# Kernel tuning notes

Measured on AMD Instinct MI355X. Metric: run time of the kernel, lower is better.

The kernel has to match this reference:

```python
import jax, jax.numpy as jnp
import numpy as np

EPS = 1e-5  # BatchNorm eps (eval mode, uses running stats)


def _conv1x1(x, W, b):
    # x: [B,C,H,W], W: [O,C], b: [O] -> [B,O,H,W]
    return jnp.einsum('bchw,oc->bohw', x, W) + b[None, :, None, None]


def setup_inputs() -> dict:
    key = jax.random.key(0)
    ks = jax.random.split(key, 13)
    B, C, M, N = 16, 512, 64, 64
    CR = C // 2
    s = 0.02
    return {
        'x': jax.random.normal(ks[0], (B, C, M, N), dtype=jnp.float32),
        'Wq': jax.random.normal(ks[1], (CR, C), dtype=jnp.float32) * s,
        'bq': jax.random.normal(ks[2], (CR,), dtype=jnp.float32) * s,
        'Wk': jax.random.normal(ks[3], (CR, C), dtype=jnp.float32) * s,
        'bk': jax.random.normal(ks[4], (CR,), dtype=jnp.float32) * s,
        'Wv': jax.random.normal(ks[5], (CR, C), dtype=jnp.float32) * s,
        'bv': jax.random.normal(ks[6], (CR,), dtype=jnp.float32) * s,
        'Wr': jax.random.normal(ks[7], (C, CR), dtype=jnp.float32) * s,
        'br': jax.random.normal(ks[8], (C,), dtype=jnp.float32) * s,
        'gamma': jax.random.normal(ks[9], (C,), dtype=jnp.float32) * 0.1 + 1.0,
        'beta': jax.random.normal(ks[10], (C,), dtype=jnp.float32) * 0.1,
        'running_mean': jax.random.normal(ks[11], (C,), dtype=jnp.float32) * 0.1,
        'running_var': jax.random.uniform(ks[12], (C,), dtype=jnp.float32, minval=0.5, maxval=1.5),
    }


def reference(x, Wq, bq, Wk, bk, Wv, bv, Wr, br, gamma, beta, running_mean, running_var):
    b, c, m, n = x.shape
    cr = Wq.shape[0]
    # 1x1-conv QKV projections
    Q = _conv1x1(x, Wq, bq).reshape(b * cr, m, n)
    K = _conv1x1(x, Wk, bk).reshape(b * cr, m, n)
    V = _conv1x1(x, Wv, bv).reshape(b * cr, m, n)
    # per-channel spatial attention over rows: [b*cr, m, m]
    corr = jnp.einsum('gik,gjk->gij', Q, K)
    attn = jax.nn.softmax(corr, axis=-1)
    y = jnp.einsum('gij,gjn->gin', attn, V).reshape(b, cr, m, n)
    # reconstruct: 1x1 conv + BatchNorm (eval mode) + residual
    y = _conv1x1(y, Wr, br)
    inv = gamma / jnp.sqrt(running_var + EPS)
    y = y * inv[None, :, None, None] + (beta - running_mean * inv)[None, :, None, None]
    return y + x
```

## Files before the change

### kernel.cpp

```cpp
#include <hip/hip_runtime.h>

typedef __attribute__((ext_vector_type(8))) short bf16x8;
typedef __attribute__((ext_vector_type(4))) float f32x4;

#define DEVI static __device__ __forceinline__

DEVI unsigned short f2b(float f) {
  union { float f; unsigned u; } v; v.f = f;
  unsigned r = v.u + 0x7fffu + ((v.u >> 16) & 1u);
  return (unsigned short)(r >> 16);
}

typedef const __attribute__((address_space(1))) void* gas1_t;
typedef __attribute__((address_space(3))) void* las3_t;
#define GL16(g, l) __builtin_amdgcn_global_load_lds((gas1_t)(g), (las3_t)(l), 16, 0, 0)

#define WAITVM(N) asm volatile("s_waitcnt vmcnt(" #N ")" ::: "memory")
#define WAITLGKM  asm volatile("s_waitcnt lgkmcnt(0)" ::: "memory")
#define SCHEDBAR  __builtin_amdgcn_sched_barrier(0)

#define OFF_WQKV  0ull
#define OFF_WR    786432ull
#define OFF_BQKV  1048576ull
#define OFF_SCALE 1051648ull
#define OFF_OFF2  1053696ull
#define OFF_XT    2097152ull
#define OFF_YT    2097152ull
#define OFF_Y     35651584ull
#define OFF_Q     69206016ull

__global__ __launch_bounds__(256) void k_xt(
    const float* __restrict__ x, unsigned short* __restrict__ xt,
    const float* __restrict__ Wq, const float* __restrict__ bq,
    const float* __restrict__ Wk, const float* __restrict__ bk,
    const float* __restrict__ Wv, const float* __restrict__ bv,
    const float* __restrict__ Wr, const float* __restrict__ br,
    const float* __restrict__ gamma, const float* __restrict__ beta,
    const float* __restrict__ rm, const float* __restrict__ rv,
    unsigned short* __restrict__ wqkv, unsigned short* __restrict__ wrb,
    float* __restrict__ bqkv, float* __restrict__ scale, float* __restrict__ off2)
{
  __shared__ unsigned short tile[64][72];
  const int t = threadIdx.x;
  const int bid = blockIdx.x + blockIdx.y * 64 + blockIdx.z * 512;

  if (bid < 1536) {
    int i = bid * 256 + t;
    if (i < 768 * 512) {
      int o = i >> 9, c = i & 511;
      float v = (o < 256) ? Wq[o * 512 + c] : (o < 512 ? Wk[(o - 256) * 512 + c] : Wv[(o - 512) * 512 + c]);
      wqkv[i] = f2b(v);
    }
    if (i < 512 * 256) wrb[i] = f2b(Wr[i]);
    if (i < 768) bqkv[i] = (i < 256) ? bq[i] : (i < 512 ? bk[i - 256] : bv[i - 512]);
    if (i < 512) {
      float inv = gamma[i] * rsqrtf(rv[i] + 1e-5f);
      scale[i] = inv;
      off2[i] = (br[i] - rm[i]) * inv + beta[i];
    }
  }

  const int b = blockIdx.z, c0 = blockIdx.y * 64, s0 = blockIdx.x * 64;
  const int r = t >> 2, cc = (t & 3) * 16;
  const float* src = x + ((size_t)b * 512 + c0 + r) * 4096 + s0 + cc;
  #pragma unroll
  for (int j = 0; j < 16; j += 4) {
    float4 v = *(const float4*)(src + j);
    tile[r][cc + j + 0] = f2b(v.x);
    tile[r][cc + j + 1] = f2b(v.y);
    tile[r][cc + j + 2] = f2b(v.z);
    tile[r][cc + j + 3] = f2b(v.w);
  }
  __syncthreads();
  unsigned short* dst = xt + ((size_t)b * 4096 + s0 + r) * 512 + c0 + cc;
  bf16x8 o0, o1;
  #pragma unroll
  for (int j = 0; j < 8; ++j) { o0[j] = tile[cc + j][r]; o1[j] = tile[cc + 8 + j][r]; }
  *(bf16x8*)(dst) = o0;
  *(bf16x8*)(dst + 8) = o1;
}

__global__ __launch_bounds__(256) void k_qkv(
    const unsigned short* __restrict__ xt, const unsigned short* __restrict__ wqkv,
    const float* __restrict__ bqkv, unsigned short* __restrict__ qkv)
{
  __shared__ unsigned short lds[2][2][8192];
  const int wg = (blockIdx.x & 7) * 384 + (blockIdx.x >> 3);
  const int o0 = (wg % 6) * 128;
  const int s0 = ((wg / 6) & 31) * 128;
  const int b  = wg / 192;
  const int t = threadIdx.x, w = t >> 6, l = t & 63;
  const int wm = w >> 1, wn = w & 1, lr = l & 15;
  const int lkE = (l >> 4) * 8;
  const int swE = (lr & 7) * 8;
  const int cp = (t & 7) ^ ((t >> 3) & 7);

  const unsigned short* Ag = wqkv + (size_t)(o0 + (t >> 3)) * 512 + cp * 8;
  const unsigned short* Bg = xt + ((size_t)b * 4096 + s0 + (t >> 3)) * 512 + cp * 8;

  const f32x4 z = {0.f, 0.f, 0.f, 0.f};
  f32x4 acc[4][4];
  #pragma unroll
  for (int i = 0; i < 4; ++i)
    #pragma unroll
    for (int j = 0; j < 4; ++j) acc[i][j] = z;

#define STG_Q(st, kt) do { \
    _Pragma("unroll") \
    for (int j = 0; j < 4; ++j) { \
      GL16(Ag + (kt) * 64 + j * 32 * 512, (char*)&lds[st][0][0] + j * 4096 + t * 16); \
      GL16(Bg + (kt) * 64 + j * 32 * 512, (char*)&lds[st][1][0] + j * 4096 + t * 16); \
    } \
  } while (0)

#define CMP_Q(st) do { \
    const unsigned short* A  = &lds[st][0][0]; \
    const unsigned short* Bl = &lds[st][1][0]; \
    bf16x8 af[2][4], bfr[2][4]; \
    _Pragma("unroll") \
    for (int kc = 0; kc < 2; ++kc) { \
      const int kidx = (kc * 32 + lkE) ^ swE; \
      _Pragma("unroll") \
      for (int mi = 0; mi < 4; ++mi) af[kc][mi] = *(const bf16x8*)(A + (wm * 64 + mi * 16 + lr) * 64 + kidx); \
      _Pragma("unroll") \
      for (int ni = 0; ni < 4; ++ni) bfr[kc][ni] = *(const bf16x8*)(Bl + (wn * 64 + ni * 16 + lr) * 64 + kidx); \
    } \
    __builtin_amdgcn_s_setprio(1); \
    _Pragma("unroll") \
    for (int kc = 0; kc < 2; ++kc) \
      _Pragma("unroll") \
      for (int mi = 0; mi < 4; ++mi) \
        _Pragma("unroll") \
        for (int ni = 0; ni < 4; ++ni) \
          acc[mi][ni] = __builtin_amdgcn_mfma_f32_16x16x32_bf16(af[kc][mi], bfr[kc][ni], acc[mi][ni], 0, 0, 0); \
    __builtin_amdgcn_s_setprio(0); \
  } while (0)

  STG_Q(0, 0); STG_Q(1, 1);
  #pragma unroll
  for (int kt = 0; kt < 7; ++kt) {
    WAITVM(8);
    __builtin_amdgcn_s_barrier(); SCHEDBAR;
    CMP_Q(kt & 1);
    __builtin_amdgcn_s_barrier(); SCHEDBAR;
    if (kt + 2 < 8) STG_Q(kt & 1, kt + 2);
  }
  WAITVM(0);
  __builtin_amdgcn_s_barrier(); SCHEDBAR;
  CMP_Q(1);

  #pragma unroll
  for (int mi = 0; mi < 4; ++mi) {
    #pragma unroll
    for (int reg = 0; reg < 4; ++reg) {
      const int o = o0 + wm * 64 + mi * 16 + (l >> 4) * 4 + reg;
      const float bias = bqkv[o];
      const size_t base = (size_t)(o >> 8) * 16777216ull + ((size_t)b * 256 + (o & 255)) * 4096;
      #pragma unroll
      for (int ni = 0; ni < 4; ++ni) {
        const int s = s0 + wn * 64 + ni * 16 + lr;
        qkv[base + s] = f2b(acc[mi][ni][reg] + bias);
      }
    }
  }
#undef STG_Q
#undef CMP_Q
}

__global__ __launch_bounds__(256) void k_attn(const unsigned short* __restrict__ qkv,
                                              unsigned short* __restrict__ yout)
{
  __shared__ unsigned short Vt[64][80];
  __shared__ unsigned short P[4][16][80];
  const int g = blockIdx.x;
  const unsigned short* qg = qkv + (size_t)g * 4096;
  const unsigned short* kg = qkv + 16777216ull + (size_t)g * 4096;
  const unsigned short* vg = qkv + 33554432ull + (size_t)g * 4096;
  const int t = threadIdx.x, w = t >> 6, l = t & 63;
  const int lr = l & 15, lk = (l >> 4) * 8;

  {
    const int j = t >> 2, c0 = (t & 3) * 16;
    bf16x8 a = *(const bf16x8*)(vg + j * 64 + c0);
    bf16x8 bb = *(const bf16x8*)(vg + j * 64 + c0 + 8);
    #pragma unroll
    for (int jj = 0; jj < 8; ++jj) { Vt[c0 + jj][j] = a[jj]; Vt[c0 + 8 + jj][j] = bb[jj]; }
  }

  const f32x4 z = {0.f, 0.f, 0.f, 0.f};
  bf16x8 qf[2];
  #pragma unroll
  for (int kc = 0; kc < 2; ++kc) qf[kc] = *(const bf16x8*)(qg + (w * 16 + lr) * 64 + kc * 32 + lk);
  f32x4 accS[4] = {z, z, z, z};
  __builtin_amdgcn_s_setprio(1);
  #pragma unroll
  for (int jt = 0; jt < 4; ++jt)
    #pragma unroll
    for (int kc = 0; kc < 2; ++kc) {
      bf16x8 kf = *(const bf16x8*)(kg + (jt * 16 + lr) * 64 + kc * 32 + lk);
      accS[jt] = __builtin_amdgcn_mfma_f32_16x16x32_bf16(qf[kc], kf, accS[jt], 0, 0, 0);
    }
  __builtin_amdgcn_s_setprio(0);

  #pragma unroll
  for (int reg = 0; reg < 4; ++reg) {
    float mx = fmaxf(fmaxf(accS[0][reg], accS[1][reg]), fmaxf(accS[2][reg], accS[3][reg]));
    #pragma unroll
    for (int m = 1; m < 16; m <<= 1) mx = fmaxf(mx, __shfl_xor(mx, m, 64));
    float e0 = __expf(accS[0][reg] - mx), e1 = __expf(accS[1][reg] - mx);
    float e2 = __expf(accS[2][reg] - mx), e3 = __expf(accS[3][reg] - mx);
    float sm = e0 + e1 + e2 + e3;
    #pragma unroll
    for (int m = 1; m < 16; m <<= 1) sm += __shfl_xor(sm, m, 64);
    const float rs = 1.f / sm;
    const int row = (l >> 4) * 4 + reg;
    P[w][row][0 * 16 + lr] = f2b(e0 * rs);
    P[w][row][1 * 16 + lr] = f2b(e1 * rs);
    P[w][row][2 * 16 + lr] = f2b(e2 * rs);
    P[w][row][3 * 16 + lr] = f2b(e3 * rs);
  }
  __syncthreads();

  bf16x8 pf[2];
  #pragma unroll
  for (int kc = 0; kc < 2; ++kc) pf[kc] = *(const bf16x8*)(&P[w][lr][kc * 32 + lk]);
  f32x4 accY[4] = {z, z, z, z};
  __builtin_amdgcn_s_setprio(1);
  #pragma unroll
  for (int nt = 0; nt < 4; ++nt)
    #pragma unroll
    for (int kc = 0; kc < 2; ++kc) {
      bf16x8 vf = *(const bf16x8*)(&Vt[nt * 16 + lr][kc * 32 + lk]);
      accY[nt] = __builtin_amdgcn_mfma_f32_16x16x32_bf16(pf[kc], vf, accY[nt], 0, 0, 0);
    }
  __builtin_amdgcn_s_setprio(0);

  unsigned short* yg = yout + (size_t)g * 4096;
  #pragma unroll
  for (int nt = 0; nt < 4; ++nt)
    #pragma unroll
    for (int reg = 0; reg < 4; ++reg) {
      const int i = w * 16 + (l >> 4) * 4 + reg;
      yg[i * 64 + nt * 16 + lr] = f2b(accY[nt][reg]);
    }
}

__global__ __launch_bounds__(256) void k_yt(const unsigned short* __restrict__ y, unsigned short* __restrict__ yt)
{
  __shared__ unsigned short tile[64][72];
  const int b = blockIdx.z, cr0 = blockIdx.y * 64, s0 = blockIdx.x * 64;
  const int t = threadIdx.x, r = t >> 2, c0 = (t & 3) * 16;
  const unsigned short* src = y + ((size_t)b * 256 + cr0 + r) * 4096 + s0 + c0;
  bf16x8 a = *(const bf16x8*)(src);
  bf16x8 bb = *(const bf16x8*)(src + 8);
  #pragma unroll
  for (int j = 0; j < 8; ++j) { tile[r][c0 + j] = a[j]; tile[r][c0 + 8 + j] = bb[j]; }
  __syncthreads();
  unsigned short* dst = yt + ((size_t)b * 4096 + s0 + r) * 256 + cr0 + c0;
  bf16x8 o0, o1;
  #pragma unroll
  for (int j = 0; j < 8; ++j) { o0[j] = tile[c0 + j][r]; o1[j] = tile[c0 + 8 + j][r]; }
  *(bf16x8*)(dst) = o0;
  *(bf16x8*)(dst + 8) = o1;
}

__global__ __launch_bounds__(256) void k_recon(
    const unsigned short* __restrict__ yt, const unsigned short* __restrict__ wrb,
    const float* __restrict__ scale, const float* __restrict__ off2,
    const float* __restrict__ x, float* __restrict__ out)
{
  __shared__ unsigned short lds[2][2][8192];
  const int wg = (blockIdx.x & 7) * 256 + (blockIdx.x >> 3);
  const int o0 = (wg % 4) * 128;
  const int s0 = ((wg / 4) & 31) * 128;
  const int b  = wg / 128;
  const int t = threadIdx.x, w = t >> 6, l = t & 63;
  const int wm = w >> 1, wn = w & 1, lr = l & 15;
  const int lkE = (l >> 4) * 8;
  const int swE = (lr & 7) * 8;
  const int cp = (t & 7) ^ ((t >> 3) & 7);

  const unsigned short* Ag = wrb + (size_t)(o0 + (t >> 3)) * 256 + cp * 8;
  const unsigned short* Bg = yt + ((size_t)b * 4096 + s0 + (t >> 3)) * 256 + cp * 8;

  const f32x4 z = {0.f, 0.f, 0.f, 0.f};
  f32x4 acc[4][4];
  #pragma unroll
  for (int i = 0; i < 4; ++i)
    #pragma unroll
    for (int j = 0; j < 4; ++j) acc[i][j] = z;

#define STG_R(st, kt) do { \
    _Pragma("unroll") \
    for (int j = 0; j < 4; ++j) { \
      GL16(Ag + (kt) * 64 + j * 32 * 256, (char*)&lds[st][0][0] + j * 4096 + t * 16); \
      GL16(Bg + (kt) * 64 + j * 32 * 256, (char*)&lds[st][1][0] + j * 4096 + t * 16); \
    } \
  } while (0)

#define CMP_R(st) do { \
    const unsigned short* A  = &lds[st][0][0]; \
    const unsigned short* Bl = &lds[st][1][0]; \
    bf16x8 af[2][4], bfr[2][4]; \
    _Pragma("unroll") \
    for (int kc = 0; kc < 2; ++kc) { \
      const int kidx = (kc * 32 + lkE) ^ swE; \
      _Pragma("unroll") \
      for (int mi = 0; mi < 4; ++mi) af[kc][mi] = *(const bf16x8*)(A + (wm * 64 + mi * 16 + lr) * 64 + kidx); \
      _Pragma("unroll") \
      for (int ni = 0; ni < 4; ++ni) bfr[kc][ni] = *(const bf16x8*)(Bl + (wn * 64 + ni * 16 + lr) * 64 + kidx); \
    } \
    __builtin_amdgcn_s_setprio(1); \
    _Pragma("unroll") \
    for (int kc = 0; kc < 2; ++kc) \
      _Pragma("unroll") \
      for (int mi = 0; mi < 4; ++mi) \
        _Pragma("unroll") \
        for (int ni = 0; ni < 4; ++ni) \
          acc[mi][ni] = __builtin_amdgcn_mfma_f32_16x16x32_bf16(af[kc][mi], bfr[kc][ni], acc[mi][ni], 0, 0, 0); \
    __builtin_amdgcn_s_setprio(0); \
  } while (0)

  STG_R(0, 0); STG_R(1, 1);
  #pragma unroll
  for (int kt = 0; kt < 3; ++kt) {
    WAITVM(8);
    __builtin_amdgcn_s_barrier(); SCHEDBAR;
    CMP_R(kt & 1);
    __builtin_amdgcn_s_barrier(); SCHEDBAR;
    if (kt + 2 < 4) STG_R(kt & 1, kt + 2);
  }
  WAITVM(0);
  __builtin_amdgcn_s_barrier(); SCHEDBAR;
  CMP_R(1);

  #pragma unroll
  for (int mi = 0; mi < 4; ++mi) {
    #pragma unroll
    for (int reg = 0; reg < 4; ++reg) {
      const int o = o0 + wm * 64 + mi * 16 + (l >> 4) * 4 + reg;
      const float sc = scale[o], of = off2[o];
      const size_t base = ((size_t)b * 512 + o) * 4096;
      #pragma unroll
      for (int ni = 0; ni < 4; ++ni) {
        const int s = s0 + wn * 64 + ni * 16 + lr;
        const size_t idx = base + s;
        out[idx] = acc[mi][ni][reg] * sc + of + x[idx];
      }
    }
  }
#undef STG_R
#undef CMP_R
}

extern "C" void kernel_launch(void* const* d_in, const int* in_sizes, int n_in,
                              void* d_out, int out_size, void* d_ws, size_t ws_size,
                              hipStream_t stream)
{
  const float* x     = (const float*)d_in[0];
  const float* Wq    = (const float*)d_in[1];
  const float* bq    = (const float*)d_in[2];
  const float* Wk    = (const float*)d_in[3];
  const float* bk    = (const float*)d_in[4];
  const float* Wv    = (const float*)d_in[5];
  const float* bv    = (const float*)d_in[6];
  const float* Wr    = (const float*)d_in[7];
  const float* br    = (const float*)d_in[8];
  const float* gamma = (const float*)d_in[9];
  const float* beta  = (const float*)d_in[10];
  const float* rm    = (const float*)d_in[11];
  const float* rv    = (const float*)d_in[12];

  char* ws = (char*)d_ws;
  unsigned short* wqkv  = (unsigned short*)(ws + OFF_WQKV);
  unsigned short* wrb   = (unsigned short*)(ws + OFF_WR);
  float* bqkv  = (float*)(ws + OFF_BQKV);
  float* scale = (float*)(ws + OFF_SCALE);
  float* off2  = (float*)(ws + OFF_OFF2);
  unsigned short* xt  = (unsigned short*)(ws + OFF_XT);
  unsigned short* yt  = (unsigned short*)(ws + OFF_YT);
  unsigned short* yb  = (unsigned short*)(ws + OFF_Y);
  unsigned short* qkv = (unsigned short*)(ws + OFF_Q);
  float* out = (float*)d_out;

  hipLaunchKernelGGL(k_xt, dim3(64, 8, 16), dim3(256), 0, stream,
                     x, xt, Wq, bq, Wk, bk, Wv, bv, Wr, br, gamma, beta, rm, rv,
                     wqkv, wrb, bqkv, scale, off2);
  hipLaunchKernelGGL(k_qkv, dim3(3072), dim3(256), 0, stream, xt, wqkv, bqkv, qkv);
  hipLaunchKernelGGL(k_attn, dim3(4096), dim3(256), 0, stream, qkv, yb);
  hipLaunchKernelGGL(k_yt, dim3(64, 4, 16), dim3(256), 0, stream, yb, yt);
  hipLaunchKernelGGL(k_recon, dim3(2048), dim3(256), 0, stream, yt, wrb, scale, off2, x, out);
}
```

Baseline: 215.3 us.

## Enlarge QKV GEMM tiles to 256x256 with 8 waves and phased pipelining

```diff
diff --git a/kernel.cpp b/kernel.cpp
--- a/kernel.cpp
+++ b/kernel.cpp
@@ -80,17 +80,15 @@
   *(bf16x8*)(dst + 8) = o1;
 }
 
-__global__ __launch_bounds__(256) void k_qkv(
+__global__ __launch_bounds__(512, 2) void k_qkv(
     const unsigned short* __restrict__ xt, const unsigned short* __restrict__ wqkv,
     const float* __restrict__ bqkv, unsigned short* __restrict__ qkv)
 {
-  __shared__ unsigned short lds[2][2][8192];
-  const int wg = (blockIdx.x & 7) * 384 + (blockIdx.x >> 3);
-  const int o0 = (wg % 6) * 128;
-  const int s0 = ((wg / 6) & 31) * 128;
-  const int b  = wg / 192;
+  __shared__ unsigned short Ab[2][16384];
+  __shared__ unsigned short Bb[2][16384];
+  const int b = blockIdx.z, o0 = blockIdx.y * 256, s0 = blockIdx.x * 256;
   const int t = threadIdx.x, w = t >> 6, l = t & 63;
-  const int wm = w >> 1, wn = w & 1, lr = l & 15;
+  const int wm = w >> 2, wn = w & 3, lr = l & 15;
   const int lkE = (l >> 4) * 8;
   const int swE = (lr & 7) * 8;
   const int cp = (t & 7) ^ ((t >> 3) & 7);
@@ -99,61 +97,70 @@
   const unsigned short* Bg = xt + ((size_t)b * 4096 + s0 + (t >> 3)) * 512 + cp * 8;
 
   const f32x4 z = {0.f, 0.f, 0.f, 0.f};
-  f32x4 acc[4][4];
-  #pragma unroll
-  for (int i = 0; i < 4; ++i)
+  f32x4 acc[8][4];
+  #pragma unroll
+  for (int i = 0; i < 8; ++i)
     #pragma unroll
     for (int j = 0; j < 4; ++j) acc[i][j] = z;
 
-#define STG_Q(st, kt) do { \
-    _Pragma("unroll") \
-    for (int j = 0; j < 4; ++j) { \
-      GL16(Ag + (kt) * 64 + j * 32 * 512, (char*)&lds[st][0][0] + j * 4096 + t * 16); \
-      GL16(Bg + (kt) * 64 + j * 32 * 512, (char*)&lds[st][1][0] + j * 4096 + t * 16); \
-    } \
+#define STG4(bn, kt, ph) do { \
+    GL16(Ag + (kt) * 64 + (size_t)(2 * (ph) + 0) * 64 * 512, (char*)&Ab[bn][0] + (2 * (ph) + 0) * 8192 + t * 16); \
+    GL16(Ag + (kt) * 64 + (size_t)(2 * (ph) + 1) * 64 * 512, (char*)&Ab[bn][0] + (2 * (ph) + 1) * 8192 + t * 16); \
+    GL16(Bg + (kt) * 64 + (size_t)(2 * (ph) + 0) * 64 * 512, (char*)&Bb[bn][0] + (2 * (ph) + 0) * 8192 + t * 16); \
+    GL16(Bg + (kt) * 64 + (size_t)(2 * (ph) + 1) * 64 * 512, (char*)&Bb[bn][0] + (2 * (ph) + 1) * 8192 + t * 16); \
   } while (0)
 
-#define CMP_Q(st) do { \
-    const unsigned short* A  = &lds[st][0][0]; \
-    const unsigned short* Bl = &lds[st][1][0]; \
-    bf16x8 af[2][4], bfr[2][4]; \
+  bf16x8 af[2][4];
+#define PHASE(bn, mh, nh, LOADA) do { \
+    bf16x8 bfr[2][2]; \
     _Pragma("unroll") \
     for (int kc = 0; kc < 2; ++kc) { \
       const int kidx = (kc * 32 + lkE) ^ swE; \
-      _Pragma("unroll") \
-      for (int mi = 0; mi < 4; ++mi) af[kc][mi] = *(const bf16x8*)(A + (wm * 64 + mi * 16 + lr) * 64 + kidx); \
-      _Pragma("unroll") \
-      for (int ni = 0; ni < 4; ++ni) bfr[kc][ni] = *(const bf16x8*)(Bl + (wn * 64 + ni * 16 + lr) * 64 + kidx); \
+      if (LOADA) { \
+        _Pragma("unroll") \
+        for (int mi4 = 0; mi4 < 4; ++mi4) \
+          af[kc][mi4] = *(const bf16x8*)(&Ab[bn][(wm * 128 + ((mh) * 4 + mi4) * 16 + lr) * 64 + kidx]); \
+      } \
+      _Pragma("unroll") \
+      for (int ni2 = 0; ni2 < 2; ++ni2) \
+        bfr[kc][ni2] = *(const bf16x8*)(&Bb[bn][(wn * 64 + ((nh) * 2 + ni2) * 16 + lr) * 64 + kidx]); \
     } \
+    WAITLGKM; SCHEDBAR; \
     __builtin_amdgcn_s_setprio(1); \
     _Pragma("unroll") \
     for (int kc = 0; kc < 2; ++kc) \
       _Pragma("unroll") \
-      for (int mi = 0; mi < 4; ++mi) \
+      for (int mi4 = 0; mi4 < 4; ++mi4) \
         _Pragma("unroll") \
-        for (int ni = 0; ni < 4; ++ni) \
-          acc[mi][ni] = __builtin_amdgcn_mfma_f32_16x16x32_bf16(af[kc][mi], bfr[kc][ni], acc[mi][ni], 0, 0, 0); \
+        for (int ni2 = 0; ni2 < 2; ++ni2) \
+          acc[(mh) * 4 + mi4][(nh) * 2 + ni2] = \
+            __builtin_amdgcn_mfma_f32_16x16x32_bf16(af[kc][mi4], bfr[kc][ni2], acc[(mh) * 4 + mi4][(nh) * 2 + ni2], 0, 0, 0); \
     __builtin_amdgcn_s_setprio(0); \
   } while (0)
 
-  STG_Q(0, 0); STG_Q(1, 1);
-  #pragma unroll
-  for (int kt = 0; kt < 7; ++kt) {
-    WAITVM(8);
-    __builtin_amdgcn_s_barrier(); SCHEDBAR;
-    CMP_Q(kt & 1);
-    __builtin_amdgcn_s_barrier(); SCHEDBAR;
-    if (kt + 2 < 8) STG_Q(kt & 1, kt + 2);
-  }
-  WAITVM(0);
-  __builtin_amdgcn_s_barrier(); SCHEDBAR;
-  CMP_Q(1);
-
-  #pragma unroll
-  for (int mi = 0; mi < 4; ++mi) {
+  STG4(0, 0, 0); STG4(0, 0, 1);
+  #pragma unroll
+  for (int kt = 0; kt < 8; ++kt) {
+    const int bn = kt & 1;
+    if (kt < 7) STG4(bn ^ 1, kt + 1, 0);
+    if (kt == 7) { WAITVM(0); } else { WAITVM(4); }
+    __builtin_amdgcn_s_barrier(); SCHEDBAR;
+    PHASE(bn, 0, 0, 1);
+    __builtin_amdgcn_s_barrier(); SCHEDBAR;
+    if (kt < 7) STG4(bn ^ 1, kt + 1, 1);
+    PHASE(bn, 0, 1, 0);
+    __builtin_amdgcn_s_barrier(); SCHEDBAR;
+    PHASE(bn, 1, 0, 1);
+    __builtin_amdgcn_s_barrier(); SCHEDBAR;
+    PHASE(bn, 1, 1, 0);
+    __builtin_amdgcn_s_barrier(); SCHEDBAR;
+  }
+
+  #pragma unroll
+  for (int mi = 0; mi < 8; ++mi) {
     #pragma unroll
     for (int reg = 0; reg < 4; ++reg) {
-      const int o = o0 + wm * 64 + mi * 16 + (l >> 4) * 4 + reg;
+      const int o = o0 + wm * 128 + mi * 16 + (l >> 4) * 4 + reg;
       const float bias = bqkv[o];
       const size_t base = (size_t)(o >> 8) * 16777216ull + ((size_t)b * 256 + (o & 255)) * 4096;
       #pragma unroll
@@ -163,8 +170,8 @@
       }
     }
   }
-#undef STG_Q
-#undef CMP_Q
+#undef STG4
+#undef PHASE
 }
 
 __global__ __launch_bounds__(256) void k_attn(const unsigned short* __restrict__ qkv,
@@ -270,10 +277,7 @@
     const float* __restrict__ x, float* __restrict__ out)
 {
   __shared__ unsigned short lds[2][2][8192];
-  const int wg = (blockIdx.x & 7) * 256 + (blockIdx.x >> 3);
-  const int o0 = (wg % 4) * 128;
-  const int s0 = ((wg / 4) & 31) * 128;
-  const int b  = wg / 128;
+  const int b = blockIdx.z, o0 = blockIdx.y * 128, s0 = blockIdx.x * 128;
   const int t = threadIdx.x, w = t >> 6, l = t & 63;
   const int wm = w >> 1, wn = w & 1, lr = l & 15;
   const int lkE = (l >> 4) * 8;
@@ -301,24 +305,21 @@
 #define CMP_R(st) do { \
     const unsigned short* A  = &lds[st][0][0]; \
     const unsigned short* Bl = &lds[st][1][0]; \
-    bf16x8 af[2][4], bfr[2][4]; \
     _Pragma("unroll") \
     for (int kc = 0; kc < 2; ++kc) { \
       const int kidx = (kc * 32 + lkE) ^ swE; \
-      _Pragma("unroll") \
-      for (int mi = 0; mi < 4; ++mi) af[kc][mi] = *(const bf16x8*)(A + (wm * 64 + mi * 16 + lr) * 64 + kidx); \
-      _Pragma("unroll") \
-      for (int ni = 0; ni < 4; ++ni) bfr[kc][ni] = *(const bf16x8*)(Bl + (wn * 64 + ni * 16 + lr) * 64 + kidx); \
-    } \
-    __builtin_amdgcn_s_setprio(1); \
-    _Pragma("unroll") \
-    for (int kc = 0; kc < 2; ++kc) \
+      bf16x8 af[4], bfr[4]; \
+      _Pragma("unroll") \
+      for (int mi = 0; mi < 4; ++mi) af[mi] = *(const bf16x8*)(A + (wm * 64 + mi * 16 + lr) * 64 + kidx); \
+      _Pragma("unroll") \
+      for (int ni = 0; ni < 4; ++ni) bfr[ni] = *(const bf16x8*)(Bl + (wn * 64 + ni * 16 + lr) * 64 + kidx); \
       _Pragma("unroll") \
       for (int mi = 0; mi < 4; ++mi) \
         _Pragma("unroll") \
         for (int ni = 0; ni < 4; ++ni) \
-          acc[mi][ni] = __builtin_amdgcn_mfma_f32_16x16x32_bf16(af[kc][mi], bfr[kc][ni], acc[mi][ni], 0, 0, 0); \
-    __builtin_amdgcn_s_setprio(0); \
+          acc[mi][ni] = __builtin_amdgcn_mfma_f32_16x16x32_bf16(af[mi], bfr[ni], acc[mi][ni], 0, 0, 0); \
+    } \
+    WAITLGKM; SCHEDBAR; \
   } while (0)
 
   STG_R(0, 0); STG_R(1, 1);
@@ -386,8 +387,8 @@
   hipLaunchKernelGGL(k_xt, dim3(64, 8, 16), dim3(256), 0, stream,
                      x, xt, Wq, bq, Wk, bk, Wv, bv, Wr, br, gamma, beta, rm, rv,
                      wqkv, wrb, bqkv, scale, off2);
-  hipLaunchKernelGGL(k_qkv, dim3(3072), dim3(256), 0, stream, xt, wqkv, bqkv, qkv);
+  hipLaunchKernelGGL(k_qkv, dim3(16, 3, 16), dim3(512), 0, stream, xt, wqkv, bqkv, qkv);
   hipLaunchKernelGGL(k_attn, dim3(4096), dim3(256), 0, stream, qkv, yb);
   hipLaunchKernelGGL(k_yt, dim3(64, 4, 16), dim3(256), 0, stream, yb, yt);
-  hipLaunchKernelGGL(k_recon, dim3(2048), dim3(256), 0, stream, yt, wrb, scale, off2, x, out);
-}
+  hipLaunchKernelGGL(k_recon, dim3(32, 4, 16), dim3(256), 0, stream, yt, wrb, scale, off2, x, out);
+}
```

New measurement: 219.8 us. 1.02x slower.
